# Kernel tuning notes

Measured on AMD Instinct MI355X. Metric: run time of the kernel, lower is better.

## Reference

```python
import jax, jax.numpy as jnp
import numpy as np

N, M, C_IN, H, E, L = 50000, 20, 32, 128, 800000, 3
BN_EPS = 1e-5


def setup_inputs() -> dict:
    key = jax.random.key(0)
    ks = iter(jax.random.split(key, 40))

    def rn(shape, scale=0.05):
        return jax.random.normal(next(ks), shape, dtype=jnp.float32) * scale

    inp = {
        "ensemble": jax.random.normal(next(ks), (N, M, C_IN), dtype=jnp.float32),
        "x": jax.random.normal(next(ks), (N, C_IN), dtype=jnp.float32),
        "edge_index": jax.random.randint(next(ks), (2, E), 0, N, dtype=jnp.int64),
        "edge_attr": jax.random.uniform(next(ks), (E, 1), dtype=jnp.float32),
        # DeepSet phi / rho
        "phi_w1": rn((C_IN, H)), "phi_b1": jnp.zeros((H,), jnp.float32),
        "phi_w2": rn((H, H)), "phi_b2": jnp.zeros((H,), jnp.float32),
        "rho_w1": rn((H, H)), "rho_b1": jnp.zeros((H,), jnp.float32),
        "rho_w2": rn((H, H)), "rho_b2": jnp.zeros((H,), jnp.float32),
        # dim_red Linear(in_channels + hidden, hidden)
        "dr_w": rn((C_IN + H, H)), "dr_b": jnp.zeros((H,), jnp.float32),
        # L stacked GINEConv layers (train_eps=True, edge_dim=1, MLP = Lin-BN-ReLU-Lin)
        "conv_eps": jnp.zeros((L,), jnp.float32),
        "edge_w": rn((L, 1, H)), "edge_b": jnp.zeros((L, H), jnp.float32),
        "mlp_w1": rn((L, H, H)), "mlp_b1": jnp.zeros((L, H), jnp.float32),
        "bn_g": jnp.ones((L, H), jnp.float32), "bn_b": jnp.zeros((L, H), jnp.float32),
        "bn_m": jnp.zeros((L, H), jnp.float32), "bn_v": jnp.ones((L, H), jnp.float32),
        "mlp_w2": rn((L, H, H)), "mlp_b2": jnp.zeros((L, H), jnp.float32),
        # aggr Linear(hidden, 2) for NormalCRPS
        "aggr_w": rn((H, 2)), "aggr_b": jnp.zeros((2,), jnp.float32),
    }
    return inp


def _gine_layer(h, src, dst, edge_attr, eps, ew, eb, w1, b1, g, b, m, v, w2, b2):
    # message: relu(x_j + Lin(edge_attr)) gathered along src, scatter-sum to dst
    msg = jax.nn.relu(h[src] + edge_attr @ ew + eb)          # [E, H]
    agg = jax.ops.segment_sum(msg, dst, num_segments=N)       # [N, H]
    z = (1.0 + eps) * h + agg
    z = z @ w1 + b1
    z = (z - m) * jax.lax.rsqrt(v + BN_EPS) * g + b            # BatchNorm1d (eval)
    z = jax.nn.relu(z)
    return z @ w2 + b2


def reference(ensemble, x, edge_index, edge_attr,
              phi_w1, phi_b1, phi_w2, phi_b2,
              rho_w1, rho_b1, rho_w2, rho_b2,
              dr_w, dr_b, conv_eps, edge_w, edge_b,
              mlp_w1, mlp_b1, bn_g, bn_b, bn_m, bn_v, mlp_w2, mlp_b2,
              aggr_w, aggr_b):
    # DeepSet encoder: phi per member, sum over members, rho
    phi = jax.nn.relu(ensemble @ phi_w1 + phi_b1) @ phi_w2 + phi_b2   # [N, M, H]
    agg = phi.sum(axis=1)                                              # [N, H]
    emb = jax.nn.relu(agg @ rho_w1 + rho_b1) @ rho_w2 + rho_b2         # [N, H]

    nf = jnp.concatenate([x, emb], axis=1) @ dr_w + dr_b               # [N, H]

    src, dst = edge_index[0], edge_index[1]
    h = nf
    for i in range(L):
        c = _gine_layer(h, src, dst, edge_attr, conv_eps[i],
                        edge_w[i], edge_b[i], mlp_w1[i], mlp_b1[i],
                        bn_g[i], bn_b[i], bn_m[i], bn_v[i],
                        mlp_w2[i], mlp_b2[i])
        h = jax.nn.relu(c) if i == 0 else h + jax.nn.relu(c)

    out = h @ aggr_w + aggr_b                                          # [N, 2]
    # PostProcess for NormalCRPS: mu unconstrained, sigma positive via softplus
    mu = out[:, 0:1]
    sigma = jax.nn.softplus(out[:, 1:2])
    return jnp.concatenate([mu, sigma], axis=1)
```

## Files before the change

### kernel.cpp

```cpp
#include <hip/hip_runtime.h>
#include <math.h>

#define N_NODES 50000
#define M_ENS   20
#define C_IN    32
#define H       128
#define E_EDGES 800000
#define L_LAYERS 3
#define BN_EPS  1e-5f

typedef unsigned short u16;
typedef unsigned int   u32;

typedef __attribute__((ext_vector_type(8))) short bf16x8;
typedef __attribute__((ext_vector_type(4))) float f32x4;

#define MFMA16(a, b, c) __builtin_amdgcn_mfma_f32_16x16x32_bf16((a), (b), (c), 0, 0, 0)

__device__ __forceinline__ float bf_lo(u32 p) {
    union { u32 u; float f; } v; v.u = p << 16; return v.f;
}
__device__ __forceinline__ float bf_hi(u32 p) {
    union { u32 u; float f; } v; v.u = p & 0xFFFF0000u; return v.f;
}
__device__ __forceinline__ u16 f2bf(float f) {
    union { float f; u32 u; } v; v.f = f;
    const u32 r = v.u + 0x7FFFu + ((v.u >> 16) & 1u);
    return (u16)(r >> 16);
}
__device__ __forceinline__ float bfu(u16 h) {
    union { u32 u; float f; } v; v.u = (u32)h << 16; return v.f;
}
__device__ __forceinline__ u32 pack2bf(float a, float b) {
    return (u32)f2bf(a) | ((u32)f2bf(b) << 16);
}

__device__ __forceinline__ void split8(const float* a, bf16x8& h, bf16x8& l) {
    #pragma unroll
    for (int j = 0; j < 8; ++j) {
        const u16 hv = f2bf(a[j]);
        h[j] = (short)hv;
        l[j] = (short)f2bf(a[j] - bfu(hv));
    }
}

__global__ __launch_bounds__(256) void k_fold(
    const float* __restrict__ w2,  const float* __restrict__ b2,
    const float* __restrict__ rw1, const float* __restrict__ rb1,
    const float* __restrict__ rw2, const float* __restrict__ rb2,
    const float* __restrict__ dr_w, const float* __restrict__ dr_b,
    float* __restrict__ Wf1, float* __restrict__ bf1,
    float* __restrict__ Wf2, float* __restrict__ bf2)
{
    const int g = blockIdx.x >> 7;
    const int j = blockIdx.x & 127;
    const int t = threadIdx.x;

    const float* A  = g ? rw2 : w2;
    const float* Bm = g ? (dr_w + C_IN * H) : rw1;

    __shared__ float s_col[H];
    if (t < H) s_col[t] = Bm[t * H + j];
    __syncthreads();

    const int r = t >> 1, q = t & 1;
    const float* arow = &A[r * H + q * 64];
    const float* cp = &s_col[q * 64];
    float acc = 0.f;
    #pragma unroll
    for (int u = 0; u < 64; u += 4) {
        const float4 av = *(const float4*)&arow[u];
        acc = fmaf(av.x, cp[u], acc);
        acc = fmaf(av.y, cp[u + 1], acc);
        acc = fmaf(av.z, cp[u + 2], acc);
        acc = fmaf(av.w, cp[u + 3], acc);
    }
    acc += __shfl_xor(acc, 1);
    if (q == 0) (g ? Wf2 : Wf1)[r * H + j] = acc;

    if (t == 0) {
        float bacc = g ? dr_b[j] : rb1[j];
        const float* bsrc = g ? rb2 : b2;
        const float scale = g ? 1.f : 20.f;
        for (int k = 0; k < H; ++k)
            bacc = fmaf(scale * bsrc[k], s_col[k], bacc);
        (g ? bf2 : bf1)[j] = bacc;
    }
}

__global__ __launch_bounds__(256) void k_pack(
    const float* __restrict__ w1, const float* __restrict__ w2,
    u16* __restrict__ wpk)
{
    const int tid = blockIdx.x * 256 + threadIdx.x;
    const int j    = tid & 7;
    const int lane = (tid >> 3) & 63;
    const int nt   = (tid >> 9) & 7;
    const int ks   = (tid >> 12) & 3;
    const int mat  = (tid >> 14) & 1;
    const int l    = tid >> 15;
    if (l >= L_LAYERS) return;

    const int k = ks * 32 + (lane >> 4) * 8 + j;
    const int n = nt * 16 + (lane & 15);
    const float* w = (mat ? w2 : w1) + (size_t)l * H * H;
    const float v = w[k * H + n];

    const u16 hi = f2bf(v);
    const float lo = v - bfu(hi);

    u16* base = wpk + ((size_t)(l * 2 + mat)) * 32768;
    const int idx = (ks * 8 + nt) * 512 + lane * 8 + j;
    base[idx] = hi;
    base[16384 + idx] = f2bf(lo);
}

#define PW1H 0
#define PW1L 4096
#define WF1H 8192
#define WF1L 24576
#define WF2H 40960
#define WF2L 57344
#define DRH  73728
#define DRL  77824
__global__ __launch_bounds__(256) void k_pack2(
    const float* __restrict__ phi_w1, const float* __restrict__ Wf1,
    const float* __restrict__ Wf2,    const float* __restrict__ dr_w,
    u16* __restrict__ pk)
{
    const int tid = blockIdx.x * 256 + threadIdx.x;
    int idx; const float* src; int bh; int bl;
    if (tid < 4096)       { idx = tid;         src = phi_w1; bh = PW1H; bl = PW1L; }
    else if (tid < 20480) { idx = tid - 4096;  src = Wf1;    bh = WF1H; bl = WF1L; }
    else if (tid < 36864) { idx = tid - 20480; src = Wf2;    bh = WF2H; bl = WF2L; }
    else if (tid < 40960) { idx = tid - 36864; src = dr_w;   bh = DRH;  bl = DRL;  }
    else return;

    const int j    = idx & 7;
    const int lane = (idx >> 3) & 63;
    const int nt   = (idx >> 9) & 7;
    const int ks   = idx >> 12;
    const int k = ks * 32 + (lane >> 4) * 8 + j;
    const int n = nt * 16 + (lane & 15);
    const float v = src[k * H + n];
    const u16 hi = f2bf(v);
    pk[bh + idx] = hi;
    pk[bl + idx] = f2bf(v - bfu(hi));
}

__global__ __launch_bounds__(256) void k_phi(
    const float* __restrict__ ensemble, const float* __restrict__ phi_b1,
    const u16* __restrict__ pk,
    u16* __restrict__ hh, u16* __restrict__ hl)
{
    const int n0 = blockIdx.x * 16;
    const int t  = threadIdx.x;
    const int lane = t & 63;
    const int w    = t >> 6;
    const int l15  = lane & 15;
    const int kl   = lane >> 4;

    bf16x8 pbh[8], pbl[8];
    #pragma unroll
    for (int nt = 0; nt < 8; ++nt) {
        pbh[nt] = *(const bf16x8*)&pk[PW1H + nt * 512 + lane * 8];
        pbl[nt] = *(const bf16x8*)&pk[PW1L + nt * 512 + lane * 8];
    }
    float b1v[8];
    #pragma unroll
    for (int nt = 0; nt < 8; ++nt) b1v[nt] = phi_b1[nt * 16 + l15];

    const float* ebase = ensemble
        + ((size_t)(n0 + w * 4 + (l15 & 3)) * M_ENS + (l15 >> 2) * 5) * C_IN
        + kl * 8;
    float4 av[5][2];
    #pragma unroll
    for (int tt = 0; tt < 5; ++tt) {
        av[tt][0] = *(const float4*)(ebase + tt * C_IN);
        av[tt][1] = *(const float4*)(ebase + tt * C_IN + 4);
    }

    float acc[4][8];
    #pragma unroll
    for (int r = 0; r < 4; ++r)
        #pragma unroll
        for (int nt = 0; nt < 8; ++nt) acc[r][nt] = 0.f;

    #pragma unroll
    for (int tt = 0; tt < 5; ++tt) {
        float a8[8] = {av[tt][0].x, av[tt][0].y, av[tt][0].z, av[tt][0].w,
                       av[tt][1].x, av[tt][1].y, av[tt][1].z, av[tt][1].w};
        bf16x8 ah, al;
        split8(a8, ah, al);
        #pragma unroll
        for (int nt = 0; nt < 8; ++nt) {
            f32x4 c = {0.f, 0.f, 0.f, 0.f};
            c = MFMA16(ah, pbh[nt], c);
            c = MFMA16(al, pbh[nt], c);
            c = MFMA16(ah, pbl[nt], c);
            #pragma unroll
            for (int r = 0; r < 4; ++r)
                acc[r][nt] += fmaxf(c[r] + b1v[nt], 0.f);
        }
    }

    #pragma unroll
    for (int r = 0; r < 4; ++r)
        #pragma unroll
        for (int nt = 0; nt < 8; ++nt) {
            float v = acc[r][nt];
            v += __shfl_xor(v, 16);
            v += __shfl_xor(v, 32);
            acc[r][nt] = v;
        }

    #pragma unroll
    for (int r = 0; r < 4; ++r) {
        if (kl == r) {
            const size_t row = (size_t)(n0 + w * 4 + r) * H;
            #pragma unroll
            for (int nt = 0; nt < 8; ++nt) {
                const float v = acc[r][nt];
                const u16 hv = f2bf(v);
                hh[row + nt * 16 + l15] = hv;
                hl[row + nt * 16 + l15] = f2bf(v - bfu(hv));
            }
        }
    }
}

__global__ __launch_bounds__(256) void k_emb2(
    const float* __restrict__ x,
    const u16* __restrict__ hh, const u16* hl,
    const float* __restrict__ bf1, const float* __restrict__ bf2,
    const u16* __restrict__ pk,
    u16* h_out)
{
    const int n0 = blockIdx.x * 16;
    const int t  = threadIdx.x;
    const int lane = t & 63;
    const int w    = t >> 6;
    const int l15  = lane & 15;
    const int kl   = lane >> 4;
    const int nt0  = w * 2, nt1 = nt0 + 1;
    const int nA   = nt0 * 16 + l15, nB = nt1 * 16 + l15;

    __shared__ __align__(16) u16 s_th[16 * 136], s_tl[16 * 136];

    const size_t arow = (size_t)(n0 + l15) * H;
    bf16x8 ah[4], al[4];
    #pragma unroll
    for (int ks = 0; ks < 4; ++ks) {
        ah[ks] = *(const bf16x8*)&hh[arow + ks * 32 + kl * 8];
        al[ks] = *(const bf16x8*)&hl[arow + ks * 32 + kl * 8];
    }
    const float* xb = x + (size_t)(n0 + l15) * C_IN + kl * 8;
    const float4 xv0 = *(const float4*)xb;
    const float4 xv1 = *(const float4*)(xb + 4);

    {
        f32x4 acc0 = {0.f, 0.f, 0.f, 0.f};
        f32x4 acc1 = {0.f, 0.f, 0.f, 0.f};
        #pragma unroll
        for (int ks = 0; ks < 4; ++ks) {
            const int bo0 = (ks * 8 + nt0) * 512 + lane * 8;
            const int bo1 = (ks * 8 + nt1) * 512 + lane * 8;
            const bf16x8 bh0 = *(const bf16x8*)&pk[WF1H + bo0];
            const bf16x8 bl0 = *(const bf16x8*)&pk[WF1L + bo0];
            const bf16x8 bh1 = *(const bf16x8*)&pk[WF1H + bo1];
            const bf16x8 bl1 = *(const bf16x8*)&pk[WF1L + bo1];
            acc0 = MFMA16(ah[ks], bh0, acc0);
            acc0 = MFMA16(al[ks], bh0, acc0);
            acc0 = MFMA16(ah[ks], bl0, acc0);
            acc1 = MFMA16(ah[ks], bh1, acc1);
            acc1 = MFMA16(al[ks], bh1, acc1);
            acc1 = MFMA16(ah[ks], bl1, acc1);
        }
        const float bA = bf1[nA], bB = bf1[nB];
        #pragma unroll
        for (int r = 0; r < 4; ++r) {
            const int m = kl * 4 + r;
            const float t0 = fmaxf(acc0[r] + bA, 0.f);
            const float t1 = fmaxf(acc1[r] + bB, 0.f);
            const u16 h0 = f2bf(t0), h1 = f2bf(t1);
            s_th[m * 136 + nA] = h0;
            s_tl[m * 136 + nA] = f2bf(t0 - bfu(h0));
            s_th[m * 136 + nB] = h1;
            s_tl[m * 136 + nB] = f2bf(t1 - bfu(h1));
        }
    }
    __syncthreads();

    {
        f32x4 acc0 = {0.f, 0.f, 0.f, 0.f};
        f32x4 acc1 = {0.f, 0.f, 0.f, 0.f};
        #pragma unroll
        for (int ks = 0; ks < 4; ++ks) {
            const int aoff = l15 * 136 + ks * 32 + kl * 8;
            const bf16x8 th = *(const bf16x8*)&s_th[aoff];
            const bf16x8 tl = *(const bf16x8*)&s_tl[aoff];
            const int bo0 = (ks * 8 + nt0) * 512 + lane * 8;
            const int bo1 = (ks * 8 + nt1) * 512 + lane * 8;
            const bf16x8 bh0 = *(const bf16x8*)&pk[WF2H + bo0];
            const bf16x8 bl0 = *(const bf16x8*)&pk[WF2L + bo0];
            const bf16x8 bh1 = *(const bf16x8*)&pk[WF2H + bo1];
            const bf16x8 bl1 = *(const bf16x8*)&pk[WF2L + bo1];
            acc0 = MFMA16(th, bh0, acc0);
            acc0 = MFMA16(tl, bh0, acc0);
            acc0 = MFMA16(th, bl0, acc0);
            acc1 = MFMA16(th, bh1, acc1);
            acc1 = MFMA16(tl, bh1, acc1);
            acc1 = MFMA16(th, bl1, acc1);
        }
        {
            float x8[8] = {xv0.x, xv0.y, xv0.z, xv0.w,
                           xv1.x, xv1.y, xv1.z, xv1.w};
            bf16x8 xh, xl;
            split8(x8, xh, xl);
            const bf16x8 dh0 = *(const bf16x8*)&pk[DRH + nt0 * 512 + lane * 8];
            const bf16x8 dl0 = *(const bf16x8*)&pk[DRL + nt0 * 512 + lane * 8];
            const bf16x8 dh1 = *(const bf16x8*)&pk[DRH + nt1 * 512 + lane * 8];
            const bf16x8 dl1 = *(const bf16x8*)&pk[DRL + nt1 * 512 + lane * 8];
            acc0 = MFMA16(xh, dh0, acc0);
            acc0 = MFMA16(xl, dh0, acc0);
            acc0 = MFMA16(xh, dl0, acc0);
            acc1 = MFMA16(xh, dh1, acc1);
            acc1 = MFMA16(xl, dh1, acc1);
            acc1 = MFMA16(xh, dl1, acc1);
        }
        const float bA = bf2[nA], bB = bf2[nB];
        #pragma unroll
        for (int r = 0; r < 4; ++r) {
            const int m = kl * 4 + r;
            h_out[(size_t)(n0 + m) * H + nA] = f2bf(acc0[r] + bA);
            h_out[(size_t)(n0 + m) * H + nB] = f2bf(acc1[r] + bB);
        }
    }
}

#define SCAN_B  256
#define SCAN_NB ((N_NODES + SCAN_B - 1) / SCAN_B)

__global__ __launch_bounds__(256) void k_count(
    const int* __restrict__ ei, int* __restrict__ deg)
{
    const int e = blockIdx.x * 256 + threadIdx.x;
    if (e >= E_EDGES) return;
    atomicAdd(&deg[ei[E_EDGES + e]], 1);
}

__global__ __launch_bounds__(256) void k_scanA(
    const int* __restrict__ deg, int* __restrict__ partial)
{
    const int b = blockIdx.x;
    const int t = threadIdx.x;
    const int i = b * SCAN_B + t;
    int v = (i < N_NODES) ? deg[i] : 0;
    #pragma unroll
    for (int s = 1; s < 64; s <<= 1) v += __shfl_xor(v, s);
    __shared__ int s_w[4];
    if ((t & 63) == 0) s_w[t >> 6] = v;
    __syncthreads();
    if (t == 0) partial[b] = s_w[0] + s_w[1] + s_w[2] + s_w[3];
}

__global__ __launch_bounds__(256) void k_scanB(
    int* __restrict__ partial)
{
    const int t = threadIdx.x;
    __shared__ int ss[256];
    const int v = (t < SCAN_NB) ? partial[t] : 0;
    ss[t] = v;
    __syncthreads();
    #pragma unroll
    for (int d = 1; d < 256; d <<= 1) {
        const int u = (t >= d) ? ss[t - d] : 0;
        __syncthreads();
        ss[t] += u;
        __syncthreads();
    }
    if (t < SCAN_NB) partial[t] = ss[t] - v;
}

__global__ __launch_bounds__(256) void k_scanC(
    const int* __restrict__ partial,
    int* __restrict__ off, int* __restrict__ cursor)
{
    const int b = blockIdx.x;
    const int t = threadIdx.x;
    const int i = b * SCAN_B + t;
    const int v = (i < N_NODES) ? off[i] : 0;
    __shared__ int ss[256];
    ss[t] = v;
    __syncthreads();
    #pragma unroll
    for (int d = 1; d < 256; d <<= 1) {
        const int u = (t >= d) ? ss[t - d] : 0;
        __syncthreads();
        ss[t] += u;
        __syncthreads();
    }
    const int excl = ss[t] - v + partial[b];
    if (i < N_NODES) { off[i] = excl; cursor[i] = excl; }
    if (b == 0 && t == 0) off[N_NODES] = E_EDGES;
}

__global__ __launch_bounds__(256) void k_fill(
    const int* __restrict__ ei, const float* __restrict__ ea,
    int* __restrict__ cursor, int2* __restrict__ csr)
{
    const int e = blockIdx.x * 256 + threadIdx.x;
    if (e >= E_EDGES) return;
    const int dst = ei[E_EDGES + e];
    const int pos = atomicAdd(&cursor[dst], 1);
    csr[pos] = make_int2(ei[e], __float_as_int(ea[e]));
}

#define NPB 8
__global__ __launch_bounds__(256) void k_layer(
    const int* __restrict__ off, const int2* __restrict__ csr,
    const u16* __restrict__ h_in, u16* __restrict__ h_out,
    const float* __restrict__ ew, const float* __restrict__ eb,
    const float* __restrict__ eps_p,
    const u16* __restrict__ wh1, const u16* __restrict__ wl1,
    const float* __restrict__ b1, const float* __restrict__ bn_g,
    const float* __restrict__ bn_b, const float* __restrict__ bn_m,
    const float* __restrict__ bn_v,
    const u16* __restrict__ wh2, const u16* __restrict__ wl2,
    const float* __restrict__ b2,
    const int first_layer, const int last_layer,
    const float* __restrict__ aw, const float* __restrict__ ab,
    float* __restrict__ out)
{
    const int n0 = blockIdx.x * NPB;
    const int t  = threadIdx.x;

    __shared__ __align__(16) u16   s_zh[16 * 136];
    __shared__ __align__(16) u16   s_zl[16 * 136];
    __shared__ __align__(16) u16   s_th[16 * 136];
    __shared__ __align__(16) u16   s_tl[16 * 136];
    __shared__ __align__(16) float s_r [NPB * 128];
    __shared__ __align__(16) float s_hd[NPB * 128];

    const float ep1 = 1.f + eps_p[0];

    {
        const int lane = t & 63;
        const int half = lane >> 5;
        const int c = (lane & 31) * 4;
        const int np = t >> 6;
        const int q = np * 2 + half;
        const int n = n0 + q;

        const float4 wv = *(const float4*)&ew[c];
        const float4 bv = *(const float4*)&eb[c];

        int i        = off[n];
        const int hi = off[n + 1];

        float ax0 = 0.f, ay0 = 0.f, az0 = 0.f, aw0 = 0.f;
        float ax1 = 0.f, ay1 = 0.f, az1 = 0.f, aw1 = 0.f;

        int2 p[8];
        bool have = (i + 7 < hi);
        if (have) {
            #pragma unroll
            for (int u = 0; u < 8; ++u) p[u] = csr[i + u];
        }
        while (have) {
            uint2 hq[8];
            #pragma unroll
            for (int u = 0; u < 8; ++u)
                hq[u] = *(const uint2*)&h_in[(size_t)p[u].x * H + c];

            const int inext = i + 8;
            const bool more = (inext + 7 < hi);

            #pragma unroll
            for (int u = 0; u < 8; ++u) {
                const float a = __int_as_float(p[u].y);
                const float h0 = bf_lo(hq[u].x), h1 = bf_hi(hq[u].x);
                const float h2 = bf_lo(hq[u].y), h3 = bf_hi(hq[u].y);
                if (u & 1) {
                    ax1 += fmaxf(fmaf(a, wv.x, h0) + bv.x, 0.f);
                    ay1 += fmaxf(fmaf(a, wv.y, h1) + bv.y, 0.f);
                    az1 += fmaxf(fmaf(a, wv.z, h2) + bv.z, 0.f);
                    aw1 += fmaxf(fmaf(a, wv.w, h3) + bv.w, 0.f);
                } else {
                    ax0 += fmaxf(fmaf(a, wv.x, h0) + bv.x, 0.f);
                    ay0 += fmaxf(fmaf(a, wv.y, h1) + bv.y, 0.f);
                    az0 += fmaxf(fmaf(a, wv.z, h2) + bv.z, 0.f);
                    aw0 += fmaxf(fmaf(a, wv.w, h3) + bv.w, 0.f);
                }
            }
            if (more) {
                #pragma unroll
                for (int u = 0; u < 8; ++u) p[u] = csr[inext + u];
            }
            i = inext;
            have = more;
        }
        for (; i < hi; ++i) {
            const int2 p0 = csr[i];
            const uint2 hq = *(const uint2*)&h_in[(size_t)p0.x * H + c];
            const float a0 = __int_as_float(p0.y);
            ax0 += fmaxf(fmaf(a0, wv.x, bf_lo(hq.x)) + bv.x, 0.f);
            ay0 += fmaxf(fmaf(a0, wv.y, bf_hi(hq.x)) + bv.y, 0.f);
            az0 += fmaxf(fmaf(a0, wv.z, bf_lo(hq.y)) + bv.z, 0.f);
            aw0 += fmaxf(fmaf(a0, wv.w, bf_hi(hq.y)) + bv.w, 0.f);
        }
        ax0 += ax1; ay0 += ay1; az0 += az1; aw0 += aw1;

        const uint2 ho = *(const uint2*)&h_in[(size_t)n * H + c];
        const float r0 = bf_lo(ho.x), r1 = bf_hi(ho.x);
        const float r2 = bf_lo(ho.y), r3 = bf_hi(ho.y);
        *(float4*)&s_r[q * 128 + c] = make_float4(r0, r1, r2, r3);

        const float z0 = fmaf(ep1, r0, ax0);
        const float z1 = fmaf(ep1, r1, ay0);
        const float z2 = fmaf(ep1, r2, az0);
        const float z3 = fmaf(ep1, r3, aw0);
        const u16 zh0 = f2bf(z0), zh1 = f2bf(z1), zh2 = f2bf(z2), zh3 = f2bf(z3);
        *(u32*)&s_zh[q * 136 + c]     = (u32)zh0 | ((u32)zh1 << 16);
        *(u32*)&s_zh[q * 136 + c + 2] = (u32)zh2 | ((u32)zh3 << 16);
        *(u32*)&s_zl[q * 136 + c]     = pack2bf(z0 - bfu(zh0), z1 - bfu(zh1));
        *(u32*)&s_zl[q * 136 + c + 2] = pack2bf(z2 - bfu(zh2), z3 - bfu(zh3));
    }
    __syncthreads();

    const int lane = t & 63;
    const int wv   = t >> 6;
    const int l15  = lane & 15;
    const int kl   = lane >> 4;
    const int nt0  = wv * 2, nt1 = wv * 2 + 1;
    const int nA   = nt0 * 16 + l15;
    const int nB   = nt1 * 16 + l15;

    {
        f32x4 acc0 = {0.f, 0.f, 0.f, 0.f};
        f32x4 acc1 = {0.f, 0.f, 0.f, 0.f};
        #pragma unroll
        for (int ks = 0; ks < 4; ++ks) {
            const int aoff = l15 * 136 + ks * 32 + kl * 8;
            const bf16x8 ah = *(const bf16x8*)&s_zh[aoff];
            const bf16x8 al = *(const bf16x8*)&s_zl[aoff];
            const int bo0 = (ks * 8 + nt0) * 512 + lane * 8;
            const int bo1 = (ks * 8 + nt1) * 512 + lane * 8;
            const bf16x8 bh0 = *(const bf16x8*)&wh1[bo0];
            const bf16x8 bl0 = *(const bf16x8*)&wl1[bo0];
            const bf16x8 bh1 = *(const bf16x8*)&wh1[bo1];
            const bf16x8 bl1 = *(const bf16x8*)&wl1[bo1];
            acc0 = MFMA16(ah, bh0, acc0);
            acc0 = MFMA16(al, bh0, acc0);
            acc0 = MFMA16(ah, bl0, acc0);
            acc1 = MFMA16(ah, bh1, acc1);
            acc1 = MFMA16(al, bh1, acc1);
            acc1 = MFMA16(ah, bl1, acc1);
        }
        const float sc0 = bn_g[nA] * rsqrtf(bn_v[nA] + BN_EPS);
        const float sh0 = fmaf(b1[nA] - bn_m[nA], sc0, bn_b[nA]);
        const float sc1 = bn_g[nB] * rsqrtf(bn_v[nB] + BN_EPS);
        const float sh1 = fmaf(b1[nB] - bn_m[nB], sc1, bn_b[nB]);

        if (kl < 2) {
            #pragma unroll
            for (int r = 0; r < 4; ++r) {
                const int m = kl * 4 + r;
                const float t0 = fmaxf(fmaf(acc0[r], sc0, sh0), 0.f);
                const float t1 = fmaxf(fmaf(acc1[r], sc1, sh1), 0.f);
                const u16 th0 = f2bf(t0), th1 = f2bf(t1);
                s_th[m * 136 + nA] = th0;
                s_tl[m * 136 + nA] = f2bf(t0 - bfu(th0));
                s_th[m * 136 + nB] = th1;
                s_tl[m * 136 + nB] = f2bf(t1 - bfu(th1));
            }
        }
    }
    __syncthreads();

    {
        f32x4 acc0 = {0.f, 0.f, 0.f, 0.f};
        f32x4 acc1 = {0.f, 0.f, 0.f, 0.f};
        #pragma unroll
        for (int ks = 0; ks < 4; ++ks) {
            const int aoff = l15 * 136 + ks * 32 + kl * 8;
            const bf16x8 ah = *(const bf16x8*)&s_th[aoff];
            const bf16x8 al = *(const bf16x8*)&s_tl[aoff];
            const int bo0 = (ks * 8 + nt0) * 512 + lane * 8;
            const int bo1 = (ks * 8 + nt1) * 512 + lane * 8;
            const bf16x8 bh0 = *(const bf16x8*)&wh2[bo0];
            const bf16x8 bl0 = *(const bf16x8*)&wl2[bo0];
            const bf16x8 bh1 = *(const bf16x8*)&wh2[bo1];
            const bf16x8 bl1 = *(const bf16x8*)&wl2[bo1];
            acc0 = MFMA16(ah, bh0, acc0);
            acc0 = MFMA16(al, bh0, acc0);
            acc0 = MFMA16(ah, bl0, acc0);
            acc1 = MFMA16(ah, bh1, acc1);
            acc1 = MFMA16(al, bh1, acc1);
            acc1 = MFMA16(ah, bl1, acc1);
        }
        const float bb0 = b2[nA];
        const float bb1 = b2[nB];

        if (kl < 2) {
            #pragma unroll
            for (int r = 0; r < 4; ++r) {
                const int m = kl * 4 + r;
                float h0 = fmaxf(acc0[r] + bb0, 0.f);
                float h1 = fmaxf(acc1[r] + bb1, 0.f);
                if (!first_layer) {
                    h0 += s_r[m * 128 + nA];
                    h1 += s_r[m * 128 + nB];
                }
                if (!last_layer) {
                    h_out[(size_t)(n0 + m) * H + nA] = f2bf(h0);
                    h_out[(size_t)(n0 + m) * H + nB] = f2bf(h1);
                } else {
                    s_hd[m * 128 + nA] = h0;
                    s_hd[m * 128 + nB] = h1;
                }
            }
        }
    }

    if (last_layer) {
        __syncthreads();
        const int jp = t & 63;  const int j0 = jp * 2;
        const int np = t >> 6;  const int na = np * 2, nb = na + 1;
        const float2 ha  = *(const float2*)&s_hd[na * 128 + j0];
        const float2 hbv = *(const float2*)&s_hd[nb * 128 + j0];
        const float2 awx = *(const float2*)&aw[j0 * 2];
        const float2 awy = *(const float2*)&aw[(j0 + 1) * 2];
        float mu_a = ha.x  * awx.x + ha.y  * awy.x;
        float sg_a = ha.x  * awx.y + ha.y  * awy.y;
        float mu_b = hbv.x * awx.x + hbv.y * awy.x;
        float sg_b = hbv.x * awx.y + hbv.y * awy.y;
        #pragma unroll
        for (int sft = 32; sft > 0; sft >>= 1) {
            mu_a += __shfl_down(mu_a, sft);
            sg_a += __shfl_down(sg_a, sft);
            mu_b += __shfl_down(mu_b, sft);
            sg_b += __shfl_down(sg_b, sft);
        }
        if (jp == 0) {
            const float o1a = sg_a + ab[1];
            const float o1b = sg_b + ab[1];
            const float spa = (o1a > 0.f) ? (o1a + log1pf(expf(-o1a)))
                                          : log1pf(expf(o1a));
            const float spb = (o1b > 0.f) ? (o1b + log1pf(expf(-o1b)))
                                          : log1pf(expf(o1b));
            out[(size_t)(n0 + na) * 2 + 0] = mu_a + ab[0];
            out[(size_t)(n0 + na) * 2 + 1] = spa;
            out[(size_t)(n0 + nb) * 2 + 0] = mu_b + ab[0];
            out[(size_t)(n0 + nb) * 2 + 1] = spb;
        }
    }
}

extern "C" void kernel_launch(void* const* d_in, const int* in_sizes, int n_in,
                              void* d_out, int out_size, void* d_ws, size_t ws_size,
                              hipStream_t stream)
{
    const float* ensemble = (const float*)d_in[0];
    const float* x        = (const float*)d_in[1];
    const int*   ei       = (const int*)d_in[2];
    const float* ea       = (const float*)d_in[3];
    const float* phi_w1   = (const float*)d_in[4];
    const float* phi_b1   = (const float*)d_in[5];
    const float* phi_w2   = (const float*)d_in[6];
    const float* phi_b2   = (const float*)d_in[7];
    const float* rho_w1   = (const float*)d_in[8];
    const float* rho_b1   = (const float*)d_in[9];
    const float* rho_w2   = (const float*)d_in[10];
    const float* rho_b2   = (const float*)d_in[11];
    const float* dr_w     = (const float*)d_in[12];
    const float* dr_b     = (const float*)d_in[13];
    const float* conv_eps = (const float*)d_in[14];
    const float* edge_w   = (const float*)d_in[15];
    const float* edge_b   = (const float*)d_in[16];
    const float* mlp_w1   = (const float*)d_in[17];
    const float* mlp_b1   = (const float*)d_in[18];
    const float* bn_g     = (const float*)d_in[19];
    const float* bn_b     = (const float*)d_in[20];
    const float* bn_m     = (const float*)d_in[21];
    const float* bn_v     = (const float*)d_in[22];
    const float* mlp_w2   = (const float*)d_in[23];
    const float* mlp_b2   = (const float*)d_in[24];
    const float* aggr_w   = (const float*)d_in[25];
    const float* aggr_b   = (const float*)d_in[26];

    float* out = (float*)d_out;

    float* Wf1     = (float*)d_ws;
    float* bf1     = Wf1 + H * H;
    float* Wf2     = bf1 + H;
    float* bf2     = Wf2 + H * H;
    int*   off     = (int*)(bf2 + H);
    int*   cursor  = off + (N_NODES + 2);
    int2*  csr     = (int2*)(cursor + N_NODES);
    u16*   h_a     = (u16*)(csr + E_EDGES);
    u16*   h_b     = h_a + (size_t)N_NODES * H;
    u16*   wpk     = h_b + (size_t)N_NODES * H;
    u16*   wpk2    = wpk + 196608;
    int*   partial = (int*)(wpk2 + 81920);

    u16*   hh      = h_b;
    u16*   hl      = h_a;

    const int eblocks = (E_EDGES + 255) / 256;

    k_fold<<<256, 256, 0, stream>>>(phi_w2, phi_b2, rho_w1, rho_b1,
                                    rho_w2, rho_b2, dr_w, dr_b,
                                    Wf1, bf1, Wf2, bf2);
    k_pack<<<384, 256, 0, stream>>>(mlp_w1, mlp_w2, wpk);
    k_pack2<<<160, 256, 0, stream>>>(phi_w1, Wf1, Wf2, dr_w, wpk2);

    k_phi<<<N_NODES / 16, 256, 0, stream>>>(ensemble, phi_b1, wpk2, hh, hl);
    k_emb2<<<N_NODES / 16, 256, 0, stream>>>(x, hh, hl, bf1, bf2, wpk2, h_a);

    hipMemsetAsync(off, 0, (N_NODES + 1) * sizeof(int), stream);
    k_count<<<eblocks, 256, 0, stream>>>(ei, off);
    k_scanA<<<SCAN_NB, 256, 0, stream>>>(off, partial);
    k_scanB<<<1, 256, 0, stream>>>(partial);
    k_scanC<<<SCAN_NB, 256, 0, stream>>>(partial, off, cursor);
    k_fill<<<eblocks, 256, 0, stream>>>(ei, ea, cursor, csr);

    u16* hin = h_a; u16* hout = h_b;
    for (int i = 0; i < L_LAYERS; ++i) {
        const u16* wh1 = wpk + ((size_t)i * 2 + 0) * 32768;
        const u16* wl1 = wh1 + 16384;
        const u16* wh2 = wpk + ((size_t)i * 2 + 1) * 32768;
        const u16* wl2 = wh2 + 16384;
        k_layer<<<N_NODES / NPB, 256, 0, stream>>>(
            off, csr, hin, hout,
            edge_w + (size_t)i * H, edge_b + (size_t)i * H, conv_eps + i,
            wh1, wl1,
            mlp_b1 + (size_t)i * H,
            bn_g + (size_t)i * H, bn_b + (size_t)i * H,
            bn_m + (size_t)i * H, bn_v + (size_t)i * H,
            wh2, wl2, mlp_b2 + (size_t)i * H,
            (i == 0) ? 1 : 0, (i == L_LAYERS - 1) ? 1 : 0,
            aggr_w, aggr_b, out);
        u16* tmp = hin; hin = hout; hout = tmp;
    }
}
```

Baseline: 632.4 us.

## Process 16 nodes per block in GINE layer and widen gather to 8 channels

The fused GINE layer kernel now handles 16 destination nodes per 256-thread block instead of 8, so all 16 rows of each 16x16 MFMA tile are real. Previously half the rows were padding and their results were discarded. Each thread now gathers 8 bf16 channels per neighbor with 16-byte loads instead of 4, and 16 threads cover one node. The epilogue reduction is rewritten to match. Shared memory is aliased to keep the footprint the same, but the grid has half as many blocks and each thread holds more live registers, which may reduce occupancy and the latency hiding available for the irregular gathers.

```diff
diff --git a/kernel.cpp b/kernel.cpp
--- a/kernel.cpp
+++ b/kernel.cpp
@@ -416,7 +416,7 @@
     csr[pos] = make_int2(ei[e], __float_as_int(ea[e]));
 }
 
-#define NPB 8
+#define NPB 16
 __global__ __launch_bounds__(256) void k_layer(
     const int* __restrict__ off, const int2* __restrict__ csr,
     const u16* __restrict__ h_in, u16* __restrict__ h_out,
@@ -435,31 +435,32 @@
     const int n0 = blockIdx.x * NPB;
     const int t  = threadIdx.x;
 
-    __shared__ __align__(16) u16   s_zh[16 * 136];
-    __shared__ __align__(16) u16   s_zl[16 * 136];
+    __shared__ __align__(16) u16   s_pool[2 * 16 * 136];
     __shared__ __align__(16) u16   s_th[16 * 136];
     __shared__ __align__(16) u16   s_tl[16 * 136];
-    __shared__ __align__(16) float s_r [NPB * 128];
-    __shared__ __align__(16) float s_hd[NPB * 128];
+    __shared__ __align__(16) float s_r [16 * 128];
+    u16* s_zh = s_pool;
+    u16* s_zl = s_pool + 16 * 136;
+    float* s_hd = (float*)s_pool;
 
     const float ep1 = 1.f + eps_p[0];
 
     {
-        const int lane = t & 63;
-        const int half = lane >> 5;
-        const int c = (lane & 31) * 4;
-        const int np = t >> 6;
-        const int q = np * 2 + half;
+        const int q = t >> 4;
+        const int c = (t & 15) * 8;
         const int n = n0 + q;
 
-        const float4 wv = *(const float4*)&ew[c];
-        const float4 bv = *(const float4*)&eb[c];
+        const float4 wv0 = *(const float4*)&ew[c];
+        const float4 wv1 = *(const float4*)&ew[c + 4];
+        const float4 bv0 = *(const float4*)&eb[c];
+        const float4 bv1 = *(const float4*)&eb[c + 4];
 
         int i        = off[n];
         const int hi = off[n + 1];
 
-        float ax0 = 0.f, ay0 = 0.f, az0 = 0.f, aw0 = 0.f;
-        float ax1 = 0.f, ay1 = 0.f, az1 = 0.f, aw1 = 0.f;
+        float a0[8], a1[8];
+        #pragma unroll
+        for (int j = 0; j < 8; ++j) { a0[j] = 0.f; a1[j] = 0.f; }
 
         int2 p[8];
         bool have = (i + 7 < hi);
@@ -468,10 +469,10 @@
             for (int u = 0; u < 8; ++u) p[u] = csr[i + u];
         }
         while (have) {
-            uint2 hq[8];
+            uint4 hq[8];
             #pragma unroll
             for (int u = 0; u < 8; ++u)
-                hq[u] = *(const uint2*)&h_in[(size_t)p[u].x * H + c];
+                hq[u] = *(const uint4*)&h_in[(size_t)p[u].x * H + c];
 
             const int inext = i + 8;
             const bool more = (inext + 7 < hi);
@@ -481,17 +482,17 @@
                 const float a = __int_as_float(p[u].y);
                 const float h0 = bf_lo(hq[u].x), h1 = bf_hi(hq[u].x);
                 const float h2 = bf_lo(hq[u].y), h3 = bf_hi(hq[u].y);
-                if (u & 1) {
-                    ax1 += fmaxf(fmaf(a, wv.x, h0) + bv.x, 0.f);
-                    ay1 += fmaxf(fmaf(a, wv.y, h1) + bv.y, 0.f);
-                    az1 += fmaxf(fmaf(a, wv.z, h2) + bv.z, 0.f);
-                    aw1 += fmaxf(fmaf(a, wv.w, h3) + bv.w, 0.f);
-                } else {
-                    ax0 += fmaxf(fmaf(a, wv.x, h0) + bv.x, 0.f);
-                    ay0 += fmaxf(fmaf(a, wv.y, h1) + bv.y, 0.f);
-                    az0 += fmaxf(fmaf(a, wv.z, h2) + bv.z, 0.f);
-                    aw0 += fmaxf(fmaf(a, wv.w, h3) + bv.w, 0.f);
-                }
+                const float h4 = bf_lo(hq[u].z), h5 = bf_hi(hq[u].z);
+                const float h6 = bf_lo(hq[u].w), h7 = bf_hi(hq[u].w);
+                float* acc = (u & 1) ? a1 : a0;
+                acc[0] += fmaxf(fmaf(a, wv0.x, h0) + bv0.x, 0.f);
+                acc[1] += fmaxf(fmaf(a, wv0.y, h1) + bv0.y, 0.f);
+                acc[2] += fmaxf(fmaf(a, wv0.z, h2) + bv0.z, 0.f);
+                acc[3] += fmaxf(fmaf(a, wv0.w, h3) + bv0.w, 0.f);
+                acc[4] += fmaxf(fmaf(a, wv1.x, h4) + bv1.x, 0.f);
+                acc[5] += fmaxf(fmaf(a, wv1.y, h5) + bv1.y, 0.f);
+                acc[6] += fmaxf(fmaf(a, wv1.z, h6) + bv1.z, 0.f);
+                acc[7] += fmaxf(fmaf(a, wv1.w, h7) + bv1.w, 0.f);
             }
             if (more) {
                 #pragma unroll
@@ -502,29 +503,38 @@
         }
         for (; i < hi; ++i) {
             const int2 p0 = csr[i];
-            const uint2 hq = *(const uint2*)&h_in[(size_t)p0.x * H + c];
-            const float a0 = __int_as_float(p0.y);
-            ax0 += fmaxf(fmaf(a0, wv.x, bf_lo(hq.x)) + bv.x, 0.f);
-            ay0 += fmaxf(fmaf(a0, wv.y, bf_hi(hq.x)) + bv.y, 0.f);
-            az0 += fmaxf(fmaf(a0, wv.z, bf_lo(hq.y)) + bv.z, 0.f);
-            aw0 += fmaxf(fmaf(a0, wv.w, bf_hi(hq.y)) + bv.w, 0.f);
-        }
-        ax0 += ax1; ay0 += ay1; az0 += az1; aw0 += aw1;
-
-        const uint2 ho = *(const uint2*)&h_in[(size_t)n * H + c];
+            const uint4 hq = *(const uint4*)&h_in[(size_t)p0.x * H + c];
+            const float a = __int_as_float(p0.y);
+            a0[0] += fmaxf(fmaf(a, wv0.x, bf_lo(hq.x)) + bv0.x, 0.f);
+            a0[1] += fmaxf(fmaf(a, wv0.y, bf_hi(hq.x)) + bv0.y, 0.f);
+            a0[2] += fmaxf(fmaf(a, wv0.z, bf_lo(hq.y)) + bv0.z, 0.f);
+            a0[3] += fmaxf(fmaf(a, wv0.w, bf_hi(hq.y)) + bv0.w, 0.f);
+            a0[4] += fmaxf(fmaf(a, wv1.x, bf_lo(hq.z)) + bv1.x, 0.f);
+            a0[5] += fmaxf(fmaf(a, wv1.y, bf_hi(hq.z)) + bv1.y, 0.f);
+            a0[6] += fmaxf(fmaf(a, wv1.z, bf_lo(hq.w)) + bv1.z, 0.f);
+            a0[7] += fmaxf(fmaf(a, wv1.w, bf_hi(hq.w)) + bv1.w, 0.f);
+        }
+        #pragma unroll
+        for (int j = 0; j < 8; ++j) a0[j] += a1[j];
+
+        const uint4 ho = *(const uint4*)&h_in[(size_t)n * H + c];
         const float r0 = bf_lo(ho.x), r1 = bf_hi(ho.x);
         const float r2 = bf_lo(ho.y), r3 = bf_hi(ho.y);
-        *(float4*)&s_r[q * 128 + c] = make_float4(r0, r1, r2, r3);
-
-        const float z0 = fmaf(ep1, r0, ax0);
-        const float z1 = fmaf(ep1, r1, ay0);
-        const float z2 = fmaf(ep1, r2, az0);
-        const float z3 = fmaf(ep1, r3, aw0);
-        const u16 zh0 = f2bf(z0), zh1 = f2bf(z1), zh2 = f2bf(z2), zh3 = f2bf(z3);
-        *(u32*)&s_zh[q * 136 + c]     = (u32)zh0 | ((u32)zh1 << 16);
-        *(u32*)&s_zh[q * 136 + c + 2] = (u32)zh2 | ((u32)zh3 << 16);
-        *(u32*)&s_zl[q * 136 + c]     = pack2bf(z0 - bfu(zh0), z1 - bfu(zh1));
-        *(u32*)&s_zl[q * 136 + c + 2] = pack2bf(z2 - bfu(zh2), z3 - bfu(zh3));
+        const float r4 = bf_lo(ho.z), r5 = bf_hi(ho.z);
+        const float r6 = bf_lo(ho.w), r7 = bf_hi(ho.w);
+        *(float4*)&s_r[q * 128 + c]     = make_float4(r0, r1, r2, r3);
+        *(float4*)&s_r[q * 128 + c + 4] = make_float4(r4, r5, r6, r7);
+
+        const float rr[8] = {r0, r1, r2, r3, r4, r5, r6, r7};
+        #pragma unroll
+        for (int k = 0; k < 4; ++k) {
+            const float za = fmaf(ep1, rr[2*k],   a0[2*k]);
+            const float zb = fmaf(ep1, rr[2*k+1], a0[2*k+1]);
+            const u16 zha = f2bf(za), zhb = f2bf(zb);
+            *(u32*)&s_zh[q * 136 + c + 2*k] = (u32)zha | ((u32)zhb << 16);
+            *(u32*)&s_zl[q * 136 + c + 2*k] =
+                pack2bf(za - bfu(zha), zb - bfu(zhb));
+        }
     }
     __syncthreads();
 
@@ -562,18 +572,16 @@
         const float sc1 = bn_g[nB] * rsqrtf(bn_v[nB] + BN_EPS);
         const float sh1 = fmaf(b1[nB] - bn_m[nB], sc1, bn_b[nB]);
 
-        if (kl < 2) {
-            #pragma unroll
-            for (int r = 0; r < 4; ++r) {
-                const int m = kl * 4 + r;
-                const float t0 = fmaxf(fmaf(acc0[r], sc0, sh0), 0.f);
-                const float t1 = fmaxf(fmaf(acc1[r], sc1, sh1), 0.f);
-                const u16 th0 = f2bf(t0), th1 = f2bf(t1);
-                s_th[m * 136 + nA] = th0;
-                s_tl[m * 136 + nA] = f2bf(t0 - bfu(th0));
-                s_th[m * 136 + nB] = th1;
-                s_tl[m * 136 + nB] = f2bf(t1 - bfu(th1));
-            }
+        #pragma unroll
+        for (int r = 0; r < 4; ++r) {
+            const int m = kl * 4 + r;
+            const float t0 = fmaxf(fmaf(acc0[r], sc0, sh0), 0.f);
+            const float t1 = fmaxf(fmaf(acc1[r], sc1, sh1), 0.f);
+            const u16 th0 = f2bf(t0), th1 = f2bf(t1);
+            s_th[m * 136 + nA] = th0;
+            s_tl[m * 136 + nA] = f2bf(t0 - bfu(th0));
+            s_th[m * 136 + nB] = th1;
+            s_tl[m * 136 + nB] = f2bf(t1 - bfu(th1));
         }
     }
     __syncthreads();
@@ -602,57 +610,48 @@
         const float bb0 = b2[nA];
         const float bb1 = b2[nB];
 
-        if (kl < 2) {
-            #pragma unroll
-            for (int r = 0; r < 4; ++r) {
-                const int m = kl * 4 + r;
-                float h0 = fmaxf(acc0[r] + bb0, 0.f);
-                float h1 = fmaxf(acc1[r] + bb1, 0.f);
-                if (!first_layer) {
-                    h0 += s_r[m * 128 + nA];
-                    h1 += s_r[m * 128 + nB];
-                }
-                if (!last_layer) {
-                    h_out[(size_t)(n0 + m) * H + nA] = f2bf(h0);
-                    h_out[(size_t)(n0 + m) * H + nB] = f2bf(h1);
-                } else {
-                    s_hd[m * 128 + nA] = h0;
-                    s_hd[m * 128 + nB] = h1;
-                }
+        #pragma unroll
+        for (int r = 0; r < 4; ++r) {
+            const int m = kl * 4 + r;
+            float h0 = fmaxf(acc0[r] + bb0, 0.f);
+            float h1 = fmaxf(acc1[r] + bb1, 0.f);
+            if (!first_layer) {
+                h0 += s_r[m * 128 + nA];
+                h1 += s_r[m * 128 + nB];
+            }
+            if (!last_layer) {
+                h_out[(size_t)(n0 + m) * H + nA] = f2bf(h0);
+                h_out[(size_t)(n0 + m) * H + nB] = f2bf(h1);
+            } else {
+                s_hd[m * 128 + nA] = h0;
+                s_hd[m * 128 + nB] = h1;
             }
         }
     }
 
     if (last_layer) {
         __syncthreads();
-        const int jp = t & 63;  const int j0 = jp * 2;
-        const int np = t >> 6;  const int na = np * 2, nb = na + 1;
-        const float2 ha  = *(const float2*)&s_hd[na * 128 + j0];
-        const float2 hbv = *(const float2*)&s_hd[nb * 128 + j0];
-        const float2 awx = *(const float2*)&aw[j0 * 2];
-        const float2 awy = *(const float2*)&aw[(j0 + 1) * 2];
-        float mu_a = ha.x  * awx.x + ha.y  * awy.x;
-        float sg_a = ha.x  * awx.y + ha.y  * awy.y;
-        float mu_b = hbv.x * awx.x + hbv.y * awy.x;
-        float sg_b = hbv.x * awx.y + hbv.y * awy.y;
-        #pragma unroll
-        for (int sft = 32; sft > 0; sft >>= 1) {
-            mu_a += __shfl_down(mu_a, sft);
-            sg_a += __shfl_down(sg_a, sft);
-            mu_b += __shfl_down(mu_b, sft);
-            sg_b += __shfl_down(sg_b, sft);
-        }
-        if (jp == 0) {
-            const float o1a = sg_a + ab[1];
-            const float o1b = sg_b + ab[1];
-            const float spa = (o1a > 0.f) ? (o1a + log1pf(expf(-o1a)))
-                                          : log1pf(expf(o1a));
-            const float spb = (o1b > 0.f) ? (o1b + log1pf(expf(-o1b)))
-                                          : log1pf(expf(o1b));
-            out[(size_t)(n0 + na) * 2 + 0] = mu_a + ab[0];
-            out[(size_t)(n0 + na) * 2 + 1] = spa;
-            out[(size_t)(n0 + nb) * 2 + 0] = mu_b + ab[0];
-            out[(size_t)(n0 + nb) * 2 + 1] = spb;
+        const int q = t >> 4;
+        const int c = (t & 15) * 8;
+        float mu = 0.f, sg = 0.f;
+        #pragma unroll
+        for (int j = 0; j < 8; ++j) {
+            const float hv = s_hd[q * 128 + c + j];
+            const float2 awj = *(const float2*)&aw[(c + j) * 2];
+            mu = fmaf(hv, awj.x, mu);
+            sg = fmaf(hv, awj.y, sg);
+        }
+        #pragma unroll
+        for (int s = 1; s < 16; s <<= 1) {
+            mu += __shfl_xor(mu, s);
+            sg += __shfl_xor(sg, s);
+        }
+        if ((t & 15) == 0) {
+            const float o1 = sg + ab[1];
+            const float sp = (o1 > 0.f) ? (o1 + log1pf(expf(-o1)))
+                                        : log1pf(expf(o1));
+            out[(size_t)(n0 + q) * 2 + 0] = mu + ab[0];
+            out[(size_t)(n0 + q) * 2 + 1] = sp;
         }
     }
 }
```

After: 594.7 us. -6.0%, faster.
